# Kernel optimization log

Hardware: AMD Instinct MI355X
Metric: run time of the kernel (lower is better)

## Reference

```python
import jax, jax.numpy as jnp
import numpy as np

KH = KW = 3  # kernel spatial size is hard-coded to 3 in the original layer


def _tdiv2(x):
    # matches tf.cast(x / 2, tf.int32): true-divide by 2, truncate toward zero
    return jnp.trunc(x * 0.5)


def setup_inputs() -> dict:
    key = jax.random.key(0)
    k1, k2, k3 = jax.random.split(key, 3)
    B, H, W, C, F = 4, 32, 32, 64, 128
    # integer-valued tensors stored as float32 (bit-serial math needs integer weights)
    inputs = jax.random.randint(k1, (B, H, W, C), 0, 16).astype(jnp.float32)
    kernel = jax.random.randint(k2, (KH, KW, C, F), -8, 8).astype(jnp.float32)
    bias = jax.random.randint(k3, (F,), -4, 4).astype(jnp.float32)
    return {"inputs": inputs, "kernel": kernel, "bias": bias, "bits": 4}


def reference(inputs, kernel, bias, bits):
    # Bit-serial conv2d, padding='same' (pad=1), activation='relu'.
    # Per (kernel position, input element, output channel) the original computes
    #   acc <- trunc((acc + x * (w mod 2) * sign(w_orig)) / 2); w <- trunc(w / 2)
    # for `bits` iterations, then sums over channels/kernel window.
    B, H, W, C = inputs.shape
    F = kernel.shape[-1]
    x = jnp.pad(inputs, ((0, 0), (1, 1), (1, 1), (0, 0)))  # 'same' padding, pad=1
    out = jnp.zeros((B, H, W, F), inputs.dtype)
    for i in range(KH):
        for j in range(KW):
            patch = x[:, i:i + H, j:j + W, :][..., None]   # [B,H,W,C,1]
            w = kernel[i, j]                               # [C,F]
            s = jnp.sign(w)                                # sign of ORIGINAL weight, fixed
            acc = jnp.zeros((B, H, W, C, F), inputs.dtype)
            ww = w
            for _ in range(bits):
                acc = _tdiv2(acc + patch * (jnp.mod(ww, 2.0) * s))
                ww = _tdiv2(ww)
            out = out + acc.sum(axis=3)                    # sum over C; kernel window summed by loop
    return jax.nn.relu(out + bias)
```

## Files before the change

kernel.cpp:

```cpp
#include <hip/hip_runtime.h>
#include <stdint.h>


typedef short s16x2 __attribute__((ext_vector_type(2)));

#define NW2 36864

__global__ __launch_bounds__(256) void prep_w(const float* __restrict__ kern,
                                              uint32_t* __restrict__ wpk) {
    int tid = blockIdx.x * 256 + threadIdx.x;
    if (tid >= NW2) return;
    int e   = tid & 3;
    int f   = (tid >> 2) & 127;
    int c8  = (tid >> 9) & 7;
    int ki  = tid >> 12;
    int c   = c8 * 8 + e * 2;
    int wlo = (int)kern[(ki * 64 + c    ) * 128 + f];
    int whi = (int)kern[(ki * 64 + c + 1) * 128 + f];
    wpk[tid] = (uint32_t)(uint16_t)(int16_t)wlo |
               ((uint32_t)(uint16_t)(int16_t)whi << 16);
}

__global__ __launch_bounds__(128, 4) void conv_main(const float* __restrict__ input,
                                                    const uint32_t* __restrict__ wpk,
                                                    const float* __restrict__ bias,
                                                    float* __restrict__ out) {
    int bid  = blockIdx.x;
    int wblk = bid & 7;
    int h    = (bid >> 3) & 31;
    int b    = bid >> 8;
    int tid  = threadIdx.x;
    int w0   = wblk * 4;

    __shared__ int patch2[3 * 6 * 32];

    for (int idx = tid; idx < 3 * 6 * 32; idx += 128) {
        int c2  = idx & 31;
        int rc  = idx >> 5;
        int r   = rc / 6;
        int col = rc - r * 6;
        int gh  = h + r - 1;
        int gw  = w0 + col - 1;
        int v = 0;
        if ((unsigned)gh < 32u && (unsigned)gw < 32u) {
            const float* p = &input[(((b * 32) + gh) * 32 + gw) * 64 + c2 * 2];
            float2 xf = *(const float2*)p;
            v = (int)xf.x | ((int)xf.y << 16);
        }
        patch2[idx] = v;
    }
    __syncthreads();

    s16x2 acc0 = {0, 0}, acc1 = {0, 0}, acc2 = {0, 0}, acc3 = {0, 0};

    #pragma unroll
    for (int i = 0; i < 3; ++i) {
        #pragma unroll
        for (int j = 0; j < 3; ++j) {
            int ki = i * 3 + j;
            const uint32_t* wrow = wpk + (size_t)(ki * 8) * 512 + tid * 4;
            const int* prw = patch2 + (i * 6 + j) * 32;
            for (int c8 = 0; c8 < 8; ++c8) {
                int4 wv = *(const int4*)(wrow + c8 * 512);
                int4 x0 = *(const int4*)(prw + c8 * 4);
                int4 x1 = *(const int4*)(prw + c8 * 4 + 32);
                int4 x2 = *(const int4*)(prw + c8 * 4 + 64);
                int4 x3 = *(const int4*)(prw + c8 * 4 + 96);
                #pragma unroll
                for (int e = 0; e < 4; ++e) {
                    s16x2 w2 = __builtin_bit_cast(s16x2, (&wv.x)[e]);
                    s16x2 A  = (w2 >> 15) & (short)15;
                    s16x2 t;
                    t = (__builtin_bit_cast(s16x2, (&x0.x)[e]) * w2 + A) >> 4; acc0 += t;
                    t = (__builtin_bit_cast(s16x2, (&x1.x)[e]) * w2 + A) >> 4; acc1 += t;
                    t = (__builtin_bit_cast(s16x2, (&x2.x)[e]) * w2 + A) >> 4; acc2 += t;
                    t = (__builtin_bit_cast(s16x2, (&x3.x)[e]) * w2 + A) >> 4; acc3 += t;
                }
            }
        }
    }

    int bi = (int)bias[tid];
    int rowbase = (b * 32 + h) * 32 + w0;
    int a;
    a = __builtin_bit_cast(int, acc0);
    { int r0 = (int)(short)a + (a >> 16) + bi; out[(rowbase + 0) * 128 + tid] = (float)(r0 < 0 ? 0 : r0); }
    a = __builtin_bit_cast(int, acc1);
    { int r1 = (int)(short)a + (a >> 16) + bi; out[(rowbase + 1) * 128 + tid] = (float)(r1 < 0 ? 0 : r1); }
    a = __builtin_bit_cast(int, acc2);
    { int r2 = (int)(short)a + (a >> 16) + bi; out[(rowbase + 2) * 128 + tid] = (float)(r2 < 0 ? 0 : r2); }
    a = __builtin_bit_cast(int, acc3);
    { int r3 = (int)(short)a + (a >> 16) + bi; out[(rowbase + 3) * 128 + tid] = (float)(r3 < 0 ? 0 : r3); }
}

extern "C" void kernel_launch(void* const* d_in, const int* in_sizes, int n_in,
                              void* d_out, int out_size, void* d_ws, size_t ws_size,
                              hipStream_t stream) {
    const float* input  = (const float*)d_in[0];
    const float* kernel = (const float*)d_in[1];
    const float* bias   = (const float*)d_in[2];

    uint32_t* wpk = (uint32_t*)d_ws;

    prep_w<<<(NW2 + 255) / 256, 256, 0, stream>>>(kernel, wpk);
    conv_main<<<1024, 128, 0, stream>>>(input, wpk, bias, (float*)d_out);
}
```

Baseline: 91.32 us.

## Prepack padded int16 input in prep kernel and halve output columns per block

The prep kernel now also converts the input into a zero-padded, int16-pair packed buffer in workspace, so conv_main no longer needs bounds checks or float-to-int conversion when staging its shared patch. Each block now computes 2 output columns instead of 4, doubling the grid to 2048 blocks, which gives more parallelism but less reuse of each weight load. The loop unrolling also changes: the c8 loop is unrolled while the i/j loops are not. The change adds an extra pass over the input through global memory.

```diff
diff --git a/kernel.cpp b/kernel.cpp
--- a/kernel.cpp
+++ b/kernel.cpp
@@ -4,93 +4,103 @@
 
 typedef short s16x2 __attribute__((ext_vector_type(2)));
 
-#define NW2 36864
+#define NWPK 36864
+#define XOFF 36864
+#define NXPK 147968
 
-__global__ __launch_bounds__(256) void prep_w(const float* __restrict__ kern,
-                                              uint32_t* __restrict__ wpk) {
-    int tid = blockIdx.x * 256 + threadIdx.x;
-    if (tid >= NW2) return;
-    int e   = tid & 3;
-    int f   = (tid >> 2) & 127;
-    int c8  = (tid >> 9) & 7;
-    int ki  = tid >> 12;
-    int c   = c8 * 8 + e * 2;
-    int wlo = (int)kern[(ki * 64 + c    ) * 128 + f];
-    int whi = (int)kern[(ki * 64 + c + 1) * 128 + f];
-    wpk[tid] = (uint32_t)(uint16_t)(int16_t)wlo |
-               ((uint32_t)(uint16_t)(int16_t)whi << 16);
+__global__ __launch_bounds__(256) void prep_all(const float* __restrict__ kern,
+                                                const float* __restrict__ input,
+                                                uint32_t* __restrict__ ws) {
+    int bid = blockIdx.x, tid = threadIdx.x;
+    if (bid < 144) {
+        int t  = bid * 256 + tid;
+        int e  = t & 3;
+        int f  = (t >> 2) & 127;
+        int c8 = (t >> 9) & 7;
+        int ki = t >> 12;
+        int c  = c8 * 8 + e * 2;
+        int wlo = (int)kern[(ki * 64 + c    ) * 128 + f];
+        int whi = (int)kern[(ki * 64 + c + 1) * 128 + f];
+        ws[t] = (uint32_t)(uint16_t)(int16_t)wlo |
+                ((uint32_t)(uint16_t)(int16_t)whi << 16);
+    } else {
+        int t = (bid - 144) * 256 + tid;
+        if (t >= NXPK) return;
+        int c2    = t & 31;
+        int rest  = t >> 5;
+        int wp    = rest % 34;
+        int rest2 = rest / 34;
+        int hp    = rest2 % 34;
+        int b     = rest2 / 34;
+        int v = 0;
+        if (hp >= 1 && hp <= 32 && wp >= 1 && wp <= 32) {
+            const float* p = &input[(((b * 32) + hp - 1) * 32 + (wp - 1)) * 64 + c2 * 2];
+            v = (int)p[0] | ((int)p[1] << 16);
+        }
+        ws[XOFF + t] = (uint32_t)v;
+    }
 }
 
-__global__ __launch_bounds__(128, 4) void conv_main(const float* __restrict__ input,
-                                                    const uint32_t* __restrict__ wpk,
+__global__ __launch_bounds__(128, 4) void conv_main(const uint32_t* __restrict__ ws,
                                                     const float* __restrict__ bias,
                                                     float* __restrict__ out) {
-    int bid  = blockIdx.x;
-    int wblk = bid & 7;
-    int h    = (bid >> 3) & 31;
-    int b    = bid >> 8;
-    int tid  = threadIdx.x;
-    int w0   = wblk * 4;
+    const uint32_t* wpk = ws;
+    const uint32_t* xpk = ws + XOFF;
 
-    __shared__ int patch2[3 * 6 * 32];
+    int bid   = blockIdx.x;
+    int wpair = bid & 15;
+    int h     = (bid >> 4) & 31;
+    int b     = bid >> 9;
+    int f     = threadIdx.x;
+    int w0    = wpair * 2;
 
-    for (int idx = tid; idx < 3 * 6 * 32; idx += 128) {
-        int c2  = idx & 31;
-        int rc  = idx >> 5;
-        int r   = rc / 6;
-        int col = rc - r * 6;
-        int gh  = h + r - 1;
-        int gw  = w0 + col - 1;
-        int v = 0;
-        if ((unsigned)gh < 32u && (unsigned)gw < 32u) {
-            const float* p = &input[(((b * 32) + gh) * 32 + gw) * 64 + c2 * 2];
-            float2 xf = *(const float2*)p;
-            v = (int)xf.x | ((int)xf.y << 16);
-        }
-        patch2[idx] = v;
+    __shared__ uint32_t patch[3 * 4 * 32];
+
+    #pragma unroll
+    for (int k = 0; k < 3; ++k) {
+        int idx  = k * 128 + f;
+        int c2   = idx & 31;
+        int colr = idx >> 5;
+        int col  = colr & 3;
+        int r    = colr >> 2;
+        patch[idx] = xpk[((b * 34 + h + r) * 34 + (w0 + col)) * 32 + c2];
     }
     __syncthreads();
 
-    s16x2 acc0 = {0, 0}, acc1 = {0, 0}, acc2 = {0, 0}, acc3 = {0, 0};
+    s16x2 acc0 = {0, 0}, acc1 = {0, 0};
 
-    #pragma unroll
     for (int i = 0; i < 3; ++i) {
-        #pragma unroll
         for (int j = 0; j < 3; ++j) {
             int ki = i * 3 + j;
-            const uint32_t* wrow = wpk + (size_t)(ki * 8) * 512 + tid * 4;
-            const int* prw = patch2 + (i * 6 + j) * 32;
+            const uint32_t* wrow = wpk + (ki * 1024 + f) * 4;
+            const uint32_t* px   = patch + (i * 4 + j) * 32;
+            #pragma unroll
             for (int c8 = 0; c8 < 8; ++c8) {
                 int4 wv = *(const int4*)(wrow + c8 * 512);
-                int4 x0 = *(const int4*)(prw + c8 * 4);
-                int4 x1 = *(const int4*)(prw + c8 * 4 + 32);
-                int4 x2 = *(const int4*)(prw + c8 * 4 + 64);
-                int4 x3 = *(const int4*)(prw + c8 * 4 + 96);
+                int4 x0 = *(const int4*)(px + c8 * 4);
+                int4 x1 = *(const int4*)(px + 32 + c8 * 4);
                 #pragma unroll
                 for (int e = 0; e < 4; ++e) {
                     s16x2 w2 = __builtin_bit_cast(s16x2, (&wv.x)[e]);
                     s16x2 A  = (w2 >> 15) & (short)15;
-                    s16x2 t;
-                    t = (__builtin_bit_cast(s16x2, (&x0.x)[e]) * w2 + A) >> 4; acc0 += t;
-                    t = (__builtin_bit_cast(s16x2, (&x1.x)[e]) * w2 + A) >> 4; acc1 += t;
-                    t = (__builtin_bit_cast(s16x2, (&x2.x)[e]) * w2 + A) >> 4; acc2 += t;
-                    t = (__builtin_bit_cast(s16x2, (&x3.x)[e]) * w2 + A) >> 4; acc3 += t;
+                    s16x2 t0 = (__builtin_bit_cast(s16x2, (&x0.x)[e]) * w2 + A) >> 4;
+                    s16x2 t1 = (__builtin_bit_cast(s16x2, (&x1.x)[e]) * w2 + A) >> 4;
+                    acc0 += t0;
+                    acc1 += t1;
                 }
             }
         }
     }
 
-    int bi = (int)bias[tid];
-    int rowbase = (b * 32 + h) * 32 + w0;
+    int bi   = (int)bias[f];
+    int base = ((b * 32 + h) * 32 + w0) * 128 + f;
     int a;
     a = __builtin_bit_cast(int, acc0);
-    { int r0 = (int)(short)a + (a >> 16) + bi; out[(rowbase + 0) * 128 + tid] = (float)(r0 < 0 ? 0 : r0); }
+    { int r0 = (int)(short)(a & 0xffff) + (a >> 16) + bi;
+      out[base]       = (float)(r0 < 0 ? 0 : r0); }
     a = __builtin_bit_cast(int, acc1);
-    { int r1 = (int)(short)a + (a >> 16) + bi; out[(rowbase + 1) * 128 + tid] = (float)(r1 < 0 ? 0 : r1); }
-    a = __builtin_bit_cast(int, acc2);
-    { int r2 = (int)(short)a + (a >> 16) + bi; out[(rowbase + 2) * 128 + tid] = (float)(r2 < 0 ? 0 : r2); }
-    a = __builtin_bit_cast(int, acc3);
-    { int r3 = (int)(short)a + (a >> 16) + bi; out[(rowbase + 3) * 128 + tid] = (float)(r3 < 0 ? 0 : r3); }
+    { int r1 = (int)(short)(a & 0xffff) + (a >> 16) + bi;
+      out[base + 128] = (float)(r1 < 0 ? 0 : r1); }
 }
 
 extern "C" void kernel_launch(void* const* d_in, const int* in_sizes, int n_in,
@@ -100,8 +110,8 @@
     const float* kernel = (const float*)d_in[1];
     const float* bias   = (const float*)d_in[2];
 
-    uint32_t* wpk = (uint32_t*)d_ws;
+    uint32_t* ws = (uint32_t*)d_ws;
 
-    prep_w<<<(NW2 + 255) / 256, 256, 0, stream>>>(kernel, wpk);
-    conv_main<<<1024, 128, 0, stream>>>(input, wpk, bias, (float*)d_out);
+    prep_all<<<144 + 579, 256, 0, stream>>>(kernel, input, ws);
+    conv_main<<<2048, 128, 0, stream>>>(ws, bias, (float*)d_out);
 }
```

New measurement: 80.97 us. -11.3%, faster.
